# Optimization experiments

Measured on AMD Instinct MI355X. Metric: run time of the kernel, lower is better.

Reference implementation:

```python
import jax, jax.numpy as jnp
import numpy as np

B, N, DIM = 2, 2048, 1024
H, DH = 16, 64
NNK = 2          # num_null_kv
SCALE = 8.0
LN_EPS = 1e-5
L2_EPS = 1e-12


def layer_norm(x, gamma):
    mu = jnp.mean(x, axis=-1, keepdims=True)
    var = jnp.var(x, axis=-1, keepdims=True)
    return (x - mu) * jax.lax.rsqrt(var + LN_EPS) * gamma  # beta buffer is zeros


def l2norm(t):
    n = jnp.sqrt(jnp.sum(t * t, axis=-1, keepdims=True))
    return t / jnp.maximum(n, L2_EPS)


def setup_inputs() -> dict:
    key = jax.random.key(0)
    ks = jax.random.split(key, 9)
    x = jax.random.normal(ks[0], (B, N, DIM), dtype=jnp.float32)
    mask = jax.random.randint(ks[1], (B, N), 0, 2).astype(bool)
    attn_bias = jax.random.normal(ks[2], (H, N, N), dtype=jnp.float32)
    gamma = jnp.ones((DIM,), dtype=jnp.float32)
    null_kv = jax.random.normal(ks[3], (H, 2 * NNK, DH), dtype=jnp.float32)
    Wq = jax.random.normal(ks[4], (DIM, H * DH), dtype=jnp.float32) * 0.02
    Wkv = jax.random.normal(ks[5], (DIM, 2 * H * DH), dtype=jnp.float32) * 0.02
    q_scale = jnp.ones((DH,), dtype=jnp.float32)
    k_scale = jnp.ones((DH,), dtype=jnp.float32)
    Wo = jax.random.normal(ks[6], (H * DH, DIM), dtype=jnp.float32) * 0.02
    return {"x": x, "mask": mask, "attn_bias": attn_bias, "gamma": gamma,
            "null_kv": null_kv, "Wq": Wq, "Wkv": Wkv,
            "q_scale": q_scale, "k_scale": k_scale, "Wo": Wo}


def reference(x, mask, attn_bias, gamma, null_kv, Wq, Wkv, q_scale, k_scale, Wo):
    b, n, dim = x.shape
    h, dh = null_kv.shape[0], null_kv.shape[-1]
    # NOTE: in the original module kv_input is captured BEFORE self.norm(x),
    # so k/v come from the un-normalized x (context=None path).
    kv_input = x
    xn = layer_norm(x, gamma)
    q = (xn @ Wq).reshape(b, n, h, dh).transpose(0, 2, 1, 3)          # b h n d
    kv = (kv_input @ Wkv).reshape(b, n, 2, h, dh)
    k = kv[:, :, 0].transpose(0, 2, 1, 3)                              # b h n d
    v = kv[:, :, 1].transpose(0, 2, 1, 3)                              # b h n d
    # null kv: 'h (n r) d -> h n r d', unbind r
    nkv = null_kv.reshape(h, NNK, 2, dh)
    nk = jnp.broadcast_to(nkv[:, :, 0][None], (b, h, NNK, dh))
    nv = jnp.broadcast_to(nkv[:, :, 1][None], (b, h, NNK, dh))
    k = jnp.concatenate([nk, k], axis=-2)                              # b h j d
    v = jnp.concatenate([nv, v], axis=-2)
    q = l2norm(q) * q_scale
    k = l2norm(k) * k_scale
    sim = jnp.einsum('bhid,bhjd->bhij', q, k) * SCALE                  # b h i j
    i, j = sim.shape[-2], sim.shape[-1]
    # attn_bias padded with num_null_kv zeros on the left of last dim
    bias = jnp.pad(attn_bias, ((0, 0), (0, 0), (NNK, 0)))
    sim = sim + bias[None]                                             # broadcast over batch
    neg = -jnp.finfo(sim.dtype).max
    # key padding mask, null kv always attendable
    m = jnp.pad(mask, ((0, 0), (NNK, 0)), constant_values=True)       # b j
    sim = jnp.where(m[:, None, None, :], sim, neg)
    # causal mask with diagonal offset j - i + 1 (null tokens always visible)
    causal = jnp.triu(jnp.ones((i, j), dtype=bool), k=j - i + 1)
    sim = jnp.where(causal, neg, sim)
    attn = jax.nn.softmax(sim, axis=-1)
    out = jnp.einsum('bhij,bhjd->bhid', attn, v)
    out = out.transpose(0, 2, 1, 3).reshape(b, n, h * dh)
    return out @ Wo
```

## Files before the change

### kernel.cpp

```cpp
#include <hip/hip_runtime.h>
#include <math.h>

typedef unsigned short ushort_t;
typedef __attribute__((ext_vector_type(8))) short bf16x8_t;
typedef __attribute__((ext_vector_type(4))) float floatx4;

typedef __attribute__((address_space(3))) unsigned int lds_uint;
typedef const __attribute__((address_space(1))) unsigned int glob_uint;

__device__ inline void gl_lds16(const ushort_t* g, ushort_t* l) {
    __builtin_amdgcn_global_load_lds((glob_uint*)g, (lds_uint*)l, 16, 0, 0);
}

__device__ inline float bf2f(ushort_t u) {
    return __uint_as_float(((unsigned int)u) << 16);
}
__device__ inline ushort_t f2bf(float f) {
    unsigned int u = __float_as_uint(f);
    unsigned int r = (u + 0x7fffu + ((u >> 16) & 1u)) >> 16;
    return (ushort_t)r;
}
__device__ inline float wave_sum(float v) {
    #pragma unroll
    for (int m = 1; m < 64; m <<= 1) v += __shfl_xor(v, m, 64);
    return v;
}

__global__ __launch_bounds__(256) void transpose_split(const float* __restrict__ W,
                                                       ushort_t* __restrict__ WTh,
                                                       ushort_t* __restrict__ WTl,
                                                       int K, int N) {
    __shared__ float t[32][33];
    int n0 = blockIdx.x * 32, k0 = blockIdx.y * 32;
    int tx = threadIdx.x, ty = threadIdx.y;
    for (int i = ty; i < 32; i += 8)
        t[i][tx] = W[(size_t)(k0 + i) * N + n0 + tx];
    __syncthreads();
    for (int i = ty; i < 32; i += 8) {
        float v = t[tx][i];
        ushort_t hv = f2bf(v);
        size_t o = (size_t)(n0 + i) * K + k0 + tx;
        WTh[o] = hv;
        WTl[o] = f2bf(v - bf2f(hv));
    }
}

__global__ __launch_bounds__(256) void ln_split(const float* __restrict__ x,
                                                const float* __restrict__ gamma,
                                                ushort_t* __restrict__ xnh,
                                                ushort_t* __restrict__ xnl,
                                                ushort_t* __restrict__ xh,
                                                ushort_t* __restrict__ xl) {
    int row = blockIdx.x, tid = threadIdx.x;
    int wid = tid >> 6, lane = tid & 63;
    float v[4];
    float s1 = 0.f, s2 = 0.f;
    #pragma unroll
    for (int i = 0; i < 4; ++i) {
        v[i] = x[(size_t)row * 1024 + tid + 256 * i];
        s1 += v[i];
        s2 += v[i] * v[i];
    }
    s1 = wave_sum(s1);
    s2 = wave_sum(s2);
    __shared__ float red[8];
    if (lane == 0) { red[wid] = s1; red[4 + wid] = s2; }
    __syncthreads();
    float S1 = red[0] + red[1] + red[2] + red[3];
    float S2 = red[4] + red[5] + red[6] + red[7];
    float mu = S1 * (1.0f / 1024.0f);
    float var = S2 * (1.0f / 1024.0f) - mu * mu;
    float rs = 1.0f / sqrtf(var + 1e-5f);
    #pragma unroll
    for (int i = 0; i < 4; ++i) {
        int c = tid + 256 * i;
        size_t o = (size_t)row * 1024 + c;
        ushort_t hx = f2bf(v[i]);
        xh[o] = hx;
        xl[o] = f2bf(v[i] - bf2f(hx));
        float xnv = (v[i] - mu) * rs * gamma[c];
        ushort_t hn = f2bf(xnv);
        xnh[o] = hn;
        xnl[o] = f2bf(xnv - bf2f(hn));
    }
}

__global__ __launch_bounds__(256) void gemm_bf3(const ushort_t* __restrict__ Ah,
                                                const ushort_t* __restrict__ Al,
                                                const ushort_t* __restrict__ Bh,
                                                const ushort_t* __restrict__ Bl,
                                                float* __restrict__ C,
                                                int M, int N, int K) {
    __shared__ ushort_t As[128 * 64];
    __shared__ ushort_t Bs[128 * 64];
    int tid = threadIdx.x;
    int w = tid >> 6, lane = tid & 63;
    int wm = w >> 1, wn = w & 1;
    int row0 = blockIdx.y * 128, col0 = blockIdx.x * 128;
    int l15 = lane & 15, l4 = lane >> 4;
    int rx = l15 & 7;
    floatx4 acc[4][4];
    #pragma unroll
    for (int i = 0; i < 4; ++i)
        #pragma unroll
        for (int j = 0; j < 4; ++j)
            #pragma unroll
            for (int v = 0; v < 4; ++v) acc[i][j][v] = 0.f;

    int nk = K >> 5;
    for (int kt = 0; kt < nk; ++kt) {
        __syncthreads();
        #pragma unroll
        for (int c = 0; c < 4; ++c) {
            int idx = c * 256 + tid;
            int r = idx >> 3, cl = idx & 7;
            int cg = cl ^ (r & 7);
            const ushort_t* ga = (cg < 4 ? Ah : Al)
                + (size_t)(row0 + r) * K + kt * 32 + (cg & 3) * 8;
            gl_lds16(ga, &As[(c * 256 + w * 64) * 8]);
            const ushort_t* gb = (cg < 4 ? Bh : Bl)
                + (size_t)(col0 + r) * K + kt * 32 + (cg & 3) * 8;
            gl_lds16(gb, &Bs[(c * 256 + w * 64) * 8]);
        }
        __syncthreads();
        bf16x8_t af_h[4], af_l[4], bf_h[4], bf_l[4];
        #pragma unroll
        for (int mi = 0; mi < 4; ++mi) {
            int r = wm * 64 + mi * 16 + l15;
            af_h[mi] = *(const bf16x8_t*)&As[(r * 8 + (l4 ^ rx)) * 8];
            af_l[mi] = *(const bf16x8_t*)&As[(r * 8 + ((4 + l4) ^ rx)) * 8];
        }
        #pragma unroll
        for (int ni = 0; ni < 4; ++ni) {
            int r = wn * 64 + ni * 16 + l15;
            bf_h[ni] = *(const bf16x8_t*)&Bs[(r * 8 + (l4 ^ rx)) * 8];
            bf_l[ni] = *(const bf16x8_t*)&Bs[(r * 8 + ((4 + l4) ^ rx)) * 8];
        }
        #pragma unroll
        for (int mi = 0; mi < 4; ++mi)
            #pragma unroll
            for (int ni = 0; ni < 4; ++ni) {
                acc[mi][ni] = __builtin_amdgcn_mfma_f32_16x16x32_bf16(
                    af_h[mi], bf_h[ni], acc[mi][ni], 0, 0, 0);
                acc[mi][ni] = __builtin_amdgcn_mfma_f32_16x16x32_bf16(
                    af_h[mi], bf_l[ni], acc[mi][ni], 0, 0, 0);
                acc[mi][ni] = __builtin_amdgcn_mfma_f32_16x16x32_bf16(
                    af_l[mi], bf_h[ni], acc[mi][ni], 0, 0, 0);
            }
    }
    #pragma unroll
    for (int mi = 0; mi < 4; ++mi)
        #pragma unroll
        for (int ni = 0; ni < 4; ++ni)
            #pragma unroll
            for (int v = 0; v < 4; ++v) {
                int rr = row0 + wm * 64 + mi * 16 + l4 * 4 + v;
                int cc = col0 + wn * 64 + ni * 16 + l15;
                C[(size_t)rr * N + cc] = acc[mi][ni][v];
            }
}

__global__ __launch_bounds__(256) void l2scale_q(const float* __restrict__ q,
                                                 const float* __restrict__ qs,
                                                 ushort_t* __restrict__ Qh,
                                                 ushort_t* __restrict__ Ql) {
    int rid = blockIdx.x * 4 + (threadIdx.x >> 6);
    int lane = threadIdx.x & 63;
    int h = rid & 15, n = (rid >> 4) & 2047, b = rid >> 15;
    float v = q[(size_t)rid * 64 + lane];
    float nrm = sqrtf(wave_sum(v * v));
    float qn = v / fmaxf(nrm, 1e-12f) * qs[lane] * 8.0f;
    size_t o = (((size_t)(b * 16 + h)) * 2048 + n) * 64 + lane;
    ushort_t hv = f2bf(qn);
    Qh[o] = hv;
    Ql[o] = f2bf(qn - bf2f(hv));
}

__global__ __launch_bounds__(256) void build_kv(const float* __restrict__ kv,
                                                const float* __restrict__ nullkv,
                                                const float* __restrict__ ks,
                                                ushort_t* __restrict__ Kh,
                                                ushort_t* __restrict__ Kl,
                                                ushort_t* __restrict__ VTh) {
    __shared__ ushort_t Vt[64][72];
    int tid = threadIdx.x;
    int w = tid >> 6, lane = tid & 63;
    int bh = blockIdx.y, b = bh >> 4, h = bh & 15;
    int j0 = blockIdx.x * 64;
    for (int jj = 0; jj < 16; ++jj) {
        int jl = w * 16 + jj;
        int j = j0 + jl;
        float kf = 0.f, vf = 0.f;
        if (j < 2) {
            kf = nullkv[(h * 4 + 2 * j) * 64 + lane];
            vf = nullkv[(h * 4 + 2 * j + 1) * 64 + lane];
        } else if (j < 2050) {
            int n = j - 2;
            size_t base = ((size_t)b * 2048 + n) * 2048;
            kf = kv[base + h * 64 + lane];
            vf = kv[base + 1024 + h * 64 + lane];
        }
        float nrm = sqrtf(wave_sum(kf * kf));
        float kn = (j < 2050) ? kf / fmaxf(nrm, 1e-12f) * ks[lane] : 0.f;
        size_t o = ((size_t)bh * 2112 + j) * 64 + lane;
        ushort_t khv = f2bf(kn);
        Kh[o] = khv;
        Kl[o] = f2bf(kn - bf2f(khv));
        Vt[jl][lane] = f2bf(vf);
    }
    __syncthreads();
    int d = tid >> 2, seg = tid & 3;
    ushort_t buf[16];
    #pragma unroll
    for (int e = 0; e < 16; ++e) buf[e] = Vt[seg * 16 + e][d];
    size_t o = ((size_t)bh * 64 + d) * 2112 + j0 + seg * 16;
    *(bf16x8_t*)&VTh[o]     = *(const bf16x8_t*)&buf[0];
    *(bf16x8_t*)&VTh[o + 8] = *(const bf16x8_t*)&buf[8];
}

__global__ __launch_bounds__(256) void attn_mfma(const ushort_t* __restrict__ Qh,
                                                 const ushort_t* __restrict__ Ql,
                                                 const ushort_t* __restrict__ Kh,
                                                 const ushort_t* __restrict__ Kl,
                                                 const ushort_t* __restrict__ VTh,
                                                 const float* __restrict__ bias,
                                                 const int* __restrict__ mask,
                                                 ushort_t* __restrict__ aoh,
                                                 ushort_t* __restrict__ aol) {
    __shared__ ushort_t Ks[2][64 * 128];
    __shared__ ushort_t Vs[2][64 * 64];
    __shared__ ushort_t Ps[4][16 * 72];

    int tid = threadIdx.x;
    int w = tid >> 6, lane = tid & 63;
    int quad = lane >> 4, l15 = lane & 15;
    int rx = l15 & 7;
    int qt = 31 - blockIdx.x;
    int bh = blockIdx.y;
    int b = bh >> 4, h = bh & 15;
    int i0 = qt * 64, r0 = i0 + w * 16;
    const int nIter = qt + 2;

    auto stage = [&](int j0, ushort_t* kd, ushort_t* vd) {
        #pragma unroll
        for (int c = 0; c < 4; ++c) {
            int idx = c * 256 + tid;
            int r = idx >> 4, cl = idx & 15;
            int cg = (cl & 8) | ((cl ^ (r & 7)) & 7);
            const ushort_t* g = ((cg & 8) ? Kl : Kh)
                + ((size_t)bh * 2112 + j0 + r) * 64 + (cg & 7) * 8;
            gl_lds16(g, &kd[(c * 256 + w * 64) * 8]);
        }
        #pragma unroll
        for (int c = 0; c < 2; ++c) {
            int idx = c * 256 + tid;
            int r = idx >> 3, cl = idx & 7;
            int cg = cl ^ (r & 7);
            const ushort_t* g = VTh + ((size_t)bh * 64 + r) * 2112 + j0 + cg * 8;
            gl_lds16(g, &vd[(c * 256 + w * 64) * 8]);
        }
    };

    float bv_n[4][4];
    int km_n[4];
    auto prefetchB = [&](int j0n) {
        #pragma unroll
        for (int jt = 0; jt < 4; ++jt) {
            int jg = j0n + jt * 16 + l15;
            km_n[jt] = (jg < 2) ? 1 : (jg < 2050 ? mask[b * 2048 + jg - 2] : 0);
            #pragma unroll
            for (int reg = 0; reg < 4; ++reg) {
                int ig = r0 + quad * 4 + reg;
                bv_n[jt][reg] = (jg >= 2 && jg < 2050)
                    ? bias[((size_t)h * 2048 + ig) * 2048 + (jg - 2)] : 0.f;
            }
        }
    };

    stage(0, Ks[0], Vs[0]);
    prefetchB(0);

    bf16x8_t aqh[2], aql[2];
    {
        size_t qbase = ((size_t)bh * 2048 + r0 + l15) * 64 + quad * 8;
        aqh[0] = *(const bf16x8_t*)&Qh[qbase];
        aqh[1] = *(const bf16x8_t*)&Qh[qbase + 32];
        aql[0] = *(const bf16x8_t*)&Ql[qbase];
        aql[1] = *(const bf16x8_t*)&Ql[qbase + 32];
    }

    floatx4 o_acc[4];
    float l_acc[4];
    #pragma unroll
    for (int dt = 0; dt < 4; ++dt)
        #pragma unroll
        for (int v = 0; v < 4; ++v) o_acc[dt][v] = 0.f;
    #pragma unroll
    for (int r = 0; r < 4; ++r) l_acc[r] = 0.f;

    __syncthreads();

    for (int it = 0; it < nIter; ++it) {
        int cur = it & 1;
        int j0 = it * 64;

        float bv[4][4];
        int km[4];
        #pragma unroll
        for (int jt = 0; jt < 4; ++jt) {
            km[jt] = km_n[jt];
            #pragma unroll
            for (int reg = 0; reg < 4; ++reg) bv[jt][reg] = bv_n[jt][reg];
        }
        if (it + 1 < nIter) {
            stage(j0 + 64, Ks[cur ^ 1], Vs[cur ^ 1]);
            prefetchB(j0 + 64);
        }
        const ushort_t* ks = Ks[cur];
        const ushort_t* vs = Vs[cur];

        floatx4 s_acc[4];
        #pragma unroll
        for (int jt = 0; jt < 4; ++jt) {
            floatx4 acc;
            #pragma unroll
            for (int v = 0; v < 4; ++v) acc[v] = 0.f;
            int r = jt * 16 + l15;
            #pragma unroll
            for (int ks2 = 0; ks2 < 2; ++ks2) {
                int cc = ks2 * 4 + quad;
                bf16x8_t kbh = *(const bf16x8_t*)&ks[(r * 16 + (cc ^ rx)) * 8];
                bf16x8_t kbl = *(const bf16x8_t*)&ks[(r * 16 + 8 + (cc ^ rx)) * 8];
                acc = __builtin_amdgcn_mfma_f32_16x16x32_bf16(aqh[ks2], kbh, acc, 0, 0, 0);
                acc = __builtin_amdgcn_mfma_f32_16x16x32_bf16(aql[ks2], kbh, acc, 0, 0, 0);
                acc = __builtin_amdgcn_mfma_f32_16x16x32_bf16(aqh[ks2], kbl, acc, 0, 0, 0);
            }
            s_acc[jt] = acc;
        }

        #pragma unroll
        for (int jt = 0; jt < 4; ++jt) {
            int jg = j0 + jt * 16 + l15;
            #pragma unroll
            for (int reg = 0; reg < 4; ++reg) {
                int ig = r0 + quad * 4 + reg;
                float sv = s_acc[jt][reg] + bv[jt][reg] - 16.0f;
                bool ok = (km[jt] != 0) && (jg <= ig + 2);
                float pv = ok ? __expf(sv) : 0.0f;
                l_acc[reg] += pv;
                Ps[w][(quad * 4 + reg) * 72 + jt * 16 + l15] = f2bf(pv);
            }
        }

        #pragma unroll
        for (int ks2 = 0; ks2 < 2; ++ks2) {
            bf16x8_t pf = *(const bf16x8_t*)&Ps[w][l15 * 72 + ks2 * 32 + quad * 8];
            #pragma unroll
            for (int dt = 0; dt < 4; ++dt) {
                int r = dt * 16 + l15;
                int cc = ks2 * 4 + quad;
                bf16x8_t vh = *(const bf16x8_t*)&vs[(r * 8 + (cc ^ rx)) * 8];
                o_acc[dt] = __builtin_amdgcn_mfma_f32_16x16x32_bf16(pf, vh, o_acc[dt], 0, 0, 0);
            }
        }

        __syncthreads();
    }

    #pragma unroll
    for (int reg = 0; reg < 4; ++reg) {
        #pragma unroll
        for (int m2 = 1; m2 < 16; m2 <<= 1)
            l_acc[reg] += __shfl_xor(l_acc[reg], m2, 64);
    }
    #pragma unroll
    for (int dt = 0; dt < 4; ++dt)
        #pragma unroll
        for (int reg = 0; reg < 4; ++reg) {
            int ig = r0 + quad * 4 + reg;
            float ov = o_acc[dt][reg] / l_acc[reg];
            size_t o = ((size_t)b * 2048 + ig) * 1024 + h * 64 + dt * 16 + l15;
            ushort_t hv = f2bf(ov);
            aoh[o] = hv;
            aol[o] = f2bf(ov - bf2f(hv));
        }
}

extern "C" void kernel_launch(void* const* d_in, const int* in_sizes, int n_in,
                              void* d_out, int out_size, void* d_ws, size_t ws_size,
                              hipStream_t stream) {
    const float* x         = (const float*)d_in[0];
    const int*   mask      = (const int*)d_in[1];
    const float* attn_bias = (const float*)d_in[2];
    const float* gamma     = (const float*)d_in[3];
    const float* null_kv   = (const float*)d_in[4];
    const float* Wq        = (const float*)d_in[5];
    const float* Wkv       = (const float*)d_in[6];
    const float* q_scale   = (const float*)d_in[7];
    const float* k_scale   = (const float*)d_in[8];
    const float* Wo        = (const float*)d_in[9];

    char* ws = (char*)d_ws;
    ushort_t* xnh   = (ushort_t*)ws; ws += (size_t)4096 * 1024 * 2;
    ushort_t* xnl   = (ushort_t*)ws; ws += (size_t)4096 * 1024 * 2;
    ushort_t* xh    = (ushort_t*)ws; ws += (size_t)4096 * 1024 * 2;
    ushort_t* xl    = (ushort_t*)ws; ws += (size_t)4096 * 1024 * 2;
    ushort_t* WqTh  = (ushort_t*)ws; ws += (size_t)1024 * 1024 * 2;
    ushort_t* WqTl  = (ushort_t*)ws; ws += (size_t)1024 * 1024 * 2;
    ushort_t* WkvTh = (ushort_t*)ws; ws += (size_t)2048 * 1024 * 2;
    ushort_t* WkvTl = (ushort_t*)ws; ws += (size_t)2048 * 1024 * 2;
    ushort_t* WoTh  = (ushort_t*)ws; ws += (size_t)1024 * 1024 * 2;
    ushort_t* WoTl  = (ushort_t*)ws; ws += (size_t)1024 * 1024 * 2;
    float*    q_ws  = (float*)ws;    ws += (size_t)4096 * 1024 * 4;
    float*    kvws  = (float*)ws;    ws += (size_t)4096 * 2048 * 4;
    ushort_t* Qh    = (ushort_t*)ws; ws += (size_t)32 * 2048 * 64 * 2;
    ushort_t* Ql    = (ushort_t*)ws; ws += (size_t)32 * 2048 * 64 * 2;
    ushort_t* Kh    = (ushort_t*)ws; ws += (size_t)32 * 2112 * 64 * 2;
    ushort_t* Kl    = (ushort_t*)ws; ws += (size_t)32 * 2112 * 64 * 2;
    ushort_t* VTh   = (ushort_t*)ws; ws += (size_t)32 * 2112 * 64 * 2;
    ushort_t* aoh   = (ushort_t*)ws; ws += (size_t)4096 * 1024 * 2;
    ushort_t* aol   = (ushort_t*)ws; ws += (size_t)4096 * 1024 * 2;

    transpose_split<<<dim3(32, 32), dim3(32, 8), 0, stream>>>(Wq, WqTh, WqTl, 1024, 1024);
    transpose_split<<<dim3(64, 32), dim3(32, 8), 0, stream>>>(Wkv, WkvTh, WkvTl, 1024, 2048);
    transpose_split<<<dim3(32, 32), dim3(32, 8), 0, stream>>>(Wo, WoTh, WoTl, 1024, 1024);
    ln_split<<<4096, 256, 0, stream>>>(x, gamma, xnh, xnl, xh, xl);
    gemm_bf3<<<dim3(8, 32), 256, 0, stream>>>(xnh, xnl, WqTh, WqTl, q_ws, 4096, 1024, 1024);
    gemm_bf3<<<dim3(16, 32), 256, 0, stream>>>(xh, xl, WkvTh, WkvTl, kvws, 4096, 2048, 1024);
    l2scale_q<<<16384, 256, 0, stream>>>(q_ws, q_scale, Qh, Ql);
    build_kv<<<dim3(33, 32), 256, 0, stream>>>(kvws, null_kv, k_scale, Kh, Kl, VTh);
    attn_mfma<<<dim3(32, 32), 256, 0, stream>>>(Qh, Ql, Kh, Kl, VTh, attn_bias, mask, aoh, aol);
    gemm_bf3<<<dim3(8, 32), 256, 0, stream>>>(aoh, aol, WoTh, WoTl, (float*)d_out, 4096, 1024, 1024);
}
```

Measured before the change: 683.1 us.

## Double-buffer GEMM tiles, load V directly to registers, fold mask into bias

The bf16x3 GEMM now double-buffers its A/B LDS tiles so the next k-tile loads while the current one computes, and it drops one barrier per iteration. In attention, the V tile is read straight from global memory into registers instead of staged through LDS. The mask and causal test are folded into the prefetched bias as a -1e30 additive term, and the exponential uses exp2 with a fused multiply-add. A launch-bounds occupancy hint of 3 blocks is added. These changes aim to hide load latency and cut LDS use and ALU work, at the cost of more GEMM LDS, uncoalesced per-lane V loads from global memory, and possible register pressure.

```diff
diff --git a/kernel.cpp b/kernel.cpp
--- a/kernel.cpp
+++ b/kernel.cpp
@@ -91,8 +91,8 @@
                                                 const ushort_t* __restrict__ Bl,
                                                 float* __restrict__ C,
                                                 int M, int N, int K) {
-    __shared__ ushort_t As[128 * 64];
-    __shared__ ushort_t Bs[128 * 64];
+    __shared__ ushort_t As[2][128 * 64];
+    __shared__ ushort_t Bs[2][128 * 64];
     int tid = threadIdx.x;
     int w = tid >> 6, lane = tid & 63;
     int wm = w >> 1, wn = w & 1;
@@ -107,9 +107,7 @@
             #pragma unroll
             for (int v = 0; v < 4; ++v) acc[i][j][v] = 0.f;
 
-    int nk = K >> 5;
-    for (int kt = 0; kt < nk; ++kt) {
-        __syncthreads();
+    auto stage = [&](int kt, int bufi) {
         #pragma unroll
         for (int c = 0; c < 4; ++c) {
             int idx = c * 256 + tid;
@@ -117,24 +115,31 @@
             int cg = cl ^ (r & 7);
             const ushort_t* ga = (cg < 4 ? Ah : Al)
                 + (size_t)(row0 + r) * K + kt * 32 + (cg & 3) * 8;
-            gl_lds16(ga, &As[(c * 256 + w * 64) * 8]);
+            gl_lds16(ga, &As[bufi][(c * 256 + w * 64) * 8]);
             const ushort_t* gb = (cg < 4 ? Bh : Bl)
                 + (size_t)(col0 + r) * K + kt * 32 + (cg & 3) * 8;
-            gl_lds16(gb, &Bs[(c * 256 + w * 64) * 8]);
-        }
-        __syncthreads();
+            gl_lds16(gb, &Bs[bufi][(c * 256 + w * 64) * 8]);
+        }
+    };
+
+    int nk = K >> 5;
+    stage(0, 0);
+    __syncthreads();
+    for (int kt = 0; kt < nk; ++kt) {
+        int cur = kt & 1;
+        if (kt + 1 < nk) stage(kt + 1, cur ^ 1);
         bf16x8_t af_h[4], af_l[4], bf_h[4], bf_l[4];
         #pragma unroll
         for (int mi = 0; mi < 4; ++mi) {
             int r = wm * 64 + mi * 16 + l15;
-            af_h[mi] = *(const bf16x8_t*)&As[(r * 8 + (l4 ^ rx)) * 8];
-            af_l[mi] = *(const bf16x8_t*)&As[(r * 8 + ((4 + l4) ^ rx)) * 8];
+            af_h[mi] = *(const bf16x8_t*)&As[cur][(r * 8 + (l4 ^ rx)) * 8];
+            af_l[mi] = *(const bf16x8_t*)&As[cur][(r * 8 + ((4 + l4) ^ rx)) * 8];
         }
         #pragma unroll
         for (int ni = 0; ni < 4; ++ni) {
             int r = wn * 64 + ni * 16 + l15;
-            bf_h[ni] = *(const bf16x8_t*)&Bs[(r * 8 + (l4 ^ rx)) * 8];
-            bf_l[ni] = *(const bf16x8_t*)&Bs[(r * 8 + ((4 + l4) ^ rx)) * 8];
+            bf_h[ni] = *(const bf16x8_t*)&Bs[cur][(r * 8 + (l4 ^ rx)) * 8];
+            bf_l[ni] = *(const bf16x8_t*)&Bs[cur][(r * 8 + ((4 + l4) ^ rx)) * 8];
         }
         #pragma unroll
         for (int mi = 0; mi < 4; ++mi)
@@ -147,6 +152,7 @@
                 acc[mi][ni] = __builtin_amdgcn_mfma_f32_16x16x32_bf16(
                     af_l[mi], bf_h[ni], acc[mi][ni], 0, 0, 0);
             }
+        __syncthreads();
     }
     #pragma unroll
     for (int mi = 0; mi < 4; ++mi)
@@ -218,17 +224,16 @@
     *(bf16x8_t*)&VTh[o + 8] = *(const bf16x8_t*)&buf[8];
 }
 
-__global__ __launch_bounds__(256) void attn_mfma(const ushort_t* __restrict__ Qh,
-                                                 const ushort_t* __restrict__ Ql,
-                                                 const ushort_t* __restrict__ Kh,
-                                                 const ushort_t* __restrict__ Kl,
-                                                 const ushort_t* __restrict__ VTh,
-                                                 const float* __restrict__ bias,
-                                                 const int* __restrict__ mask,
-                                                 ushort_t* __restrict__ aoh,
-                                                 ushort_t* __restrict__ aol) {
+__global__ __launch_bounds__(256, 3) void attn_mfma(const ushort_t* __restrict__ Qh,
+                                                    const ushort_t* __restrict__ Ql,
+                                                    const ushort_t* __restrict__ Kh,
+                                                    const ushort_t* __restrict__ Kl,
+                                                    const ushort_t* __restrict__ VTh,
+                                                    const float* __restrict__ bias,
+                                                    const int* __restrict__ mask,
+                                                    ushort_t* __restrict__ aoh,
+                                                    ushort_t* __restrict__ aol) {
     __shared__ ushort_t Ks[2][64 * 128];
-    __shared__ ushort_t Vs[2][64 * 64];
     __shared__ ushort_t Ps[4][16 * 72];
 
     int tid = threadIdx.x;
@@ -241,7 +246,7 @@
     int i0 = qt * 64, r0 = i0 + w * 16;
     const int nIter = qt + 2;
 
-    auto stage = [&](int j0, ushort_t* kd, ushort_t* vd) {
+    auto stageK = [&](int j0, ushort_t* kd) {
         #pragma unroll
         for (int c = 0; c < 4; ++c) {
             int idx = c * 256 + tid;
@@ -251,33 +256,26 @@
                 + ((size_t)bh * 2112 + j0 + r) * 64 + (cg & 7) * 8;
             gl_lds16(g, &kd[(c * 256 + w * 64) * 8]);
         }
-        #pragma unroll
-        for (int c = 0; c < 2; ++c) {
-            int idx = c * 256 + tid;
-            int r = idx >> 3, cl = idx & 7;
-            int cg = cl ^ (r & 7);
-            const ushort_t* g = VTh + ((size_t)bh * 64 + r) * 2112 + j0 + cg * 8;
-            gl_lds16(g, &vd[(c * 256 + w * 64) * 8]);
-        }
     };
 
     float bv_n[4][4];
-    int km_n[4];
     auto prefetchB = [&](int j0n) {
         #pragma unroll
         for (int jt = 0; jt < 4; ++jt) {
             int jg = j0n + jt * 16 + l15;
-            km_n[jt] = (jg < 2) ? 1 : (jg < 2050 ? mask[b * 2048 + jg - 2] : 0);
+            int km = (jg < 2) ? 1 : (jg < 2050 ? mask[b * 2048 + jg - 2] : 0);
             #pragma unroll
             for (int reg = 0; reg < 4; ++reg) {
                 int ig = r0 + quad * 4 + reg;
-                bv_n[jt][reg] = (jg >= 2 && jg < 2050)
+                float bvv = (jg >= 2 && jg < 2050)
                     ? bias[((size_t)h * 2048 + ig) * 2048 + (jg - 2)] : 0.f;
+                bool ok = (km != 0) && (jg <= ig + 2);
+                bv_n[jt][reg] = ok ? (bvv - 16.0f) * 1.442695041f : -1e30f;
             }
         }
     };
 
-    stage(0, Ks[0], Vs[0]);
+    stageK(0, Ks[0]);
     prefetchB(0);
 
     bf16x8_t aqh[2], aql[2];
@@ -298,26 +296,32 @@
     #pragma unroll
     for (int r = 0; r < 4; ++r) l_acc[r] = 0.f;
 
+    const ushort_t* vb = VTh + (size_t)bh * 64 * 2112;
+
     __syncthreads();
 
     for (int it = 0; it < nIter; ++it) {
         int cur = it & 1;
         int j0 = it * 64;
 
+        bf16x8_t vfr[2][4];
+        #pragma unroll
+        for (int ks2 = 0; ks2 < 2; ++ks2)
+            #pragma unroll
+            for (int dt = 0; dt < 4; ++dt)
+                vfr[ks2][dt] = *(const bf16x8_t*)
+                    &vb[(size_t)(dt * 16 + l15) * 2112 + j0 + ks2 * 32 + quad * 8];
+
         float bv[4][4];
-        int km[4];
-        #pragma unroll
-        for (int jt = 0; jt < 4; ++jt) {
-            km[jt] = km_n[jt];
+        #pragma unroll
+        for (int jt = 0; jt < 4; ++jt)
             #pragma unroll
             for (int reg = 0; reg < 4; ++reg) bv[jt][reg] = bv_n[jt][reg];
-        }
         if (it + 1 < nIter) {
-            stage(j0 + 64, Ks[cur ^ 1], Vs[cur ^ 1]);
+            stageK(j0 + 64, Ks[cur ^ 1]);
             prefetchB(j0 + 64);
         }
         const ushort_t* ks = Ks[cur];
-        const ushort_t* vs = Vs[cur];
 
         floatx4 s_acc[4];
         #pragma unroll
@@ -340,13 +344,9 @@
 
         #pragma unroll
         for (int jt = 0; jt < 4; ++jt) {
-            int jg = j0 + jt * 16 + l15;
             #pragma unroll
             for (int reg = 0; reg < 4; ++reg) {
-                int ig = r0 + quad * 4 + reg;
-                float sv = s_acc[jt][reg] + bv[jt][reg] - 16.0f;
-                bool ok = (km[jt] != 0) && (jg <= ig + 2);
-                float pv = ok ? __expf(sv) : 0.0f;
+                float pv = exp2f(fmaf(s_acc[jt][reg], 1.442695041f, bv[jt][reg]));
                 l_acc[reg] += pv;
                 Ps[w][(quad * 4 + reg) * 72 + jt * 16 + l15] = f2bf(pv);
             }
@@ -356,12 +356,9 @@
         for (int ks2 = 0; ks2 < 2; ++ks2) {
             bf16x8_t pf = *(const bf16x8_t*)&Ps[w][l15 * 72 + ks2 * 32 + quad * 8];
             #pragma unroll
-            for (int dt = 0; dt < 4; ++dt) {
-                int r = dt * 16 + l15;
-                int cc = ks2 * 4 + quad;
-                bf16x8_t vh = *(const bf16x8_t*)&vs[(r * 8 + (cc ^ rx)) * 8];
-                o_acc[dt] = __builtin_amdgcn_mfma_f32_16x16x32_bf16(pf, vh, o_acc[dt], 0, 0, 0);
-            }
+            for (int dt = 0; dt < 4; ++dt)
+                o_acc[dt] = __builtin_amdgcn_mfma_f32_16x16x32_bf16(
+                    pf, vfr[ks2][dt], o_acc[dt], 0, 0, 0);
         }
 
         __syncthreads();
```

After: 1.109 ms. 62.3% more time.
